# Optimization experiments

Measured on AMD Instinct MI355X. Metric: run time of the kernel, lower is better.

The kernel has to match this reference:

```python
import jax, jax.numpy as jnp
import numpy as np

HID = 256  # hardcoded LSTM hidden size in the module


def _lstm_cell(x, h, c, W_ih, W_hh, b_ih, b_hh):
    # PyTorch gate order: i, f, g, o. x,h: [1,HID]; W_*: [4H,HID]; b_*: [4H]
    gates = x @ W_ih.T + h @ W_hh.T + b_ih + b_hh  # [1,4H]
    i, f, g, o = jnp.split(gates, 4, axis=-1)
    c_new = jax.nn.sigmoid(f) * c + jax.nn.sigmoid(i) * jnp.tanh(g)
    h_new = jax.nn.sigmoid(o) * jnp.tanh(c_new)
    return h_new, c_new


def setup_inputs() -> dict:
    key = jax.random.key(0)
    ks = jax.random.split(key, 9)
    s = 0.05
    return {
        "zm_1": jax.random.normal(ks[0], (1, HID), jnp.float32) * s,
        "W_ih": jax.random.normal(ks[1], (4 * HID, HID), jnp.float32) * s,
        "W_hh": jax.random.normal(ks[2], (4 * HID, HID), jnp.float32) * s,
        "b_ih": jax.random.normal(ks[3], (4 * HID,), jnp.float32) * s,
        "b_hh": jax.random.normal(ks[4], (4 * HID,), jnp.float32) * s,
        "W_loc": jax.random.normal(ks[5], (64, HID), jnp.float32) * s,
        "b_loc": jax.random.normal(ks[6], (64,), jnp.float32) * s,
        "W_scale": jax.random.normal(ks[7], (64, HID), jnp.float32) * s,
        "b_scale": jax.random.normal(ks[8], (64,), jnp.float32) * s,
        "K": 7,
        "batch_size": 32768,
    }


def reference(zm_1, W_ih, W_hh, b_ih, b_hh, W_loc, b_loc, W_scale, b_scale, K, batch_size):
    zm_size = W_loc.shape[0]
    h0 = jnp.zeros((1, HID), zm_1.dtype)
    c0 = jnp.zeros((1, HID), zm_1.dtype)

    def step(carry, _):
        x, h, c = carry
        h_new, c_new = _lstm_cell(x, h, c, W_ih, W_hh, b_ih, b_hh)
        # LSTM output z == h_new; it is also the next step's input
        return (h_new, h_new, c_new), h_new

    _, zs = jax.lax.scan(step, (zm_1, h0, c0), None, length=K - 1)  # [K-1,1,HID]
    p_z = jnp.concatenate([zm_1[None], zs], axis=0).reshape(K, HID)  # [K,HID]

    loc = p_z @ W_loc.T + b_loc        # [K,zm]
    scale = p_z @ W_scale.T + b_scale  # [K,zm]
    # repeat over batch dim -> [K*batch_size, zm]
    loc = jnp.broadcast_to(loc[:, None, :], (K, batch_size, zm_size)).reshape(-1, zm_size)
    scale = jnp.broadcast_to(scale[:, None, :], (K, batch_size, zm_size)).reshape(-1, zm_size)
    return loc, scale
```

## Files before the change

### kernel.cpp

```cpp
#include <hip/hip_runtime.h>
#include <cstdint>
#include <cstddef>

#define HID    256
#define NROW   1024
#define KSTEPS 7
#define ZM     64
#define BATCH  32768

typedef float f32x4 __attribute__((ext_vector_type(4)));

#define WS_GATES 0
#define WS_C     (6 * NROW)
#define WS_PZ    (6 * NROW + 7 * HID)
#define WS_TAB   (6 * NROW + 14 * HID)
#define WS_WSUM  (6 * NROW + 14 * HID + 896)

__device__ __forceinline__ float sigf(float x)       { return 1.0f / (1.0f + __expf(-x)); }
__device__ __forceinline__ float tanhf_fast(float x) { return 1.0f - 2.0f / (__expf(2.0f * x) + 1.0f); }

__device__ __forceinline__ float dot4(f32x4 a, f32x4 b) {
    return a.x * b.x + a.y * b.y + a.z * b.z + a.w * b.w;
}

__global__ __launch_bounds__(256) void init_kernel(
    const float* __restrict__ zm1,
    const float* __restrict__ Wih, const float* __restrict__ Whh,
    const float* __restrict__ bih, const float* __restrict__ bhh,
    float* __restrict__ ws)
{
    const int t = threadIdx.x, b = blockIdx.x;
    f32x4*       wsum4 = (f32x4*)(ws + WS_WSUM);
    const f32x4* a4    = (const f32x4*)Wih;
    const f32x4* c4    = (const f32x4*)Whh;
    const int id = b * 256 + t;
    wsum4[id] = a4[id] + c4[id];

    if (b == 0) {
        ws[WS_PZ + t] = zm1[t];
        ws[WS_C + t]  = 0.0f;
    }
    if (b < 64) {
        const int row = b * 16 + (t >> 4);
        const int l16 = t & 15;
        const f32x4* w4 = (const f32x4*)(Wih + (size_t)row * HID);
        const f32x4* x4 = (const f32x4*)zm1;
        float part = 0.f;
        #pragma unroll
        for (int kk = 0; kk < 4; ++kk) part += dot4(w4[l16 * 4 + kk], x4[l16 * 4 + kk]);
        part += __shfl_xor(part, 1);
        part += __shfl_xor(part, 2);
        part += __shfl_xor(part, 4);
        part += __shfl_xor(part, 8);
        if (l16 == 0) ws[WS_GATES + row] = part + bih[row] + bhh[row];
    }
}

__global__ __launch_bounds__(256) void step_kernel(
    const float* __restrict__ bih, const float* __restrict__ bhh,
    float* __restrict__ ws, int s)
{
    __shared__ float hsh[HID];
    const int t = threadIdx.x, b = blockIdx.x;
    {
        const float* gp = ws + WS_GATES + (size_t)(s - 1) * NROW;
        float gi = gp[t], gf = gp[HID + t], gg = gp[2 * HID + t], go = gp[3 * HID + t];
        float cp = ws[WS_C + (size_t)(s - 1) * HID + t];
        float cn = sigf(gf) * cp + sigf(gi) * tanhf_fast(gg);
        float h  = sigf(go) * tanhf_fast(cn);
        ws[WS_C + (size_t)s * HID + t] = cn;
        if (b == 0) ws[WS_PZ + (size_t)s * HID + t] = h;
        hsh[t] = h;
    }
    __syncthreads();
    const int row = b * 16 + (t >> 4);
    const int l16 = t & 15;
    const f32x4* w4 = (const f32x4*)(ws + WS_WSUM + (size_t)row * HID);
    const f32x4* h4 = (const f32x4*)hsh;
    float part = 0.f;
    #pragma unroll
    for (int kk = 0; kk < 4; ++kk) part += dot4(w4[l16 * 4 + kk], h4[l16 * 4 + kk]);
    part += __shfl_xor(part, 1);
    part += __shfl_xor(part, 2);
    part += __shfl_xor(part, 4);
    part += __shfl_xor(part, 8);
    if (l16 == 0) ws[WS_GATES + (size_t)s * NROW + row] = part + bih[row] + bhh[row];
}

__global__ __launch_bounds__(256) void final_kernel(
    const float* __restrict__ Wloc, const float* __restrict__ bloc,
    const float* __restrict__ Wsc,  const float* __restrict__ bsc,
    float* __restrict__ ws)
{
    __shared__ float hsh[HID];
    const int t = threadIdx.x, b = blockIdx.x;
    {
        const float* gp = ws + WS_GATES + (size_t)5 * NROW;
        float gi = gp[t], gf = gp[HID + t], gg = gp[2 * HID + t], go = gp[3 * HID + t];
        float cp = ws[WS_C + (size_t)5 * HID + t];
        float cn = sigf(gf) * cp + sigf(gi) * tanhf_fast(gg);
        hsh[t] = sigf(go) * tanhf_fast(cn);
    }
    __syncthreads();
    const int wm    = b;
    const int which = wm / KSTEPS;
    const int m     = wm % KSTEPS;
    const int j     = t >> 2;
    const int q     = t & 3;
    const float* W  = which ? Wsc : Wloc;
    const float  bb = which ? bsc[j] : bloc[j];
    const f32x4* w4 = (const f32x4*)(W + (size_t)j * HID);
    const f32x4* p4 = (m == 6) ? (const f32x4*)hsh
                               : (const f32x4*)(ws + WS_PZ + (size_t)m * HID);
    float acc = 0.f;
    #pragma unroll
    for (int kk = 0; kk < 16; ++kk) acc += dot4(w4[q * 16 + kk], p4[q * 16 + kk]);
    acc += __shfl_xor(acc, 1);
    acc += __shfl_xor(acc, 2);
    if (q == 0) ws[WS_TAB + wm * ZM + j] = acc + bb;
}

__global__ __launch_bounds__(256) void bcast_kernel(
    const float* __restrict__ tab, f32x4* __restrict__ out)
{
    const int bid   = blockIdx.x;
    const int wm    = bid >> 7;
    const int chunk = bid & 127;
    const f32x4* t4 = (const f32x4*)tab;
    const f32x4 v = t4[wm * 16 + (threadIdx.x & 15)];
    size_t base = (size_t)wm * (BATCH * ZM / 4) + (size_t)chunk * 4096 + threadIdx.x;
    #pragma unroll
    for (int k = 0; k < 16; ++k) {
        __builtin_nontemporal_store(v, &out[base + (size_t)k * 256]);
    }
}

extern "C" void kernel_launch(void* const* d_in, const int* in_sizes, int n_in,
                              void* d_out, int out_size, void* d_ws, size_t ws_size,
                              hipStream_t stream) {
    const float* zm1  = (const float*)d_in[0];
    const float* Wih  = (const float*)d_in[1];
    const float* Whh  = (const float*)d_in[2];
    const float* bih  = (const float*)d_in[3];
    const float* bhh  = (const float*)d_in[4];
    const float* Wloc = (const float*)d_in[5];
    const float* bloc = (const float*)d_in[6];
    const float* Wsc  = (const float*)d_in[7];
    const float* bsc  = (const float*)d_in[8];
    float* ws = (float*)d_ws;

    init_kernel<<<256, 256, 0, stream>>>(zm1, Wih, Whh, bih, bhh, ws);
    for (int s = 1; s <= 5; ++s)
        step_kernel<<<64, 256, 0, stream>>>(bih, bhh, ws, s);
    final_kernel<<<14, 256, 0, stream>>>(Wloc, bloc, Wsc, bsc, ws);
    bcast_kernel<<<14 * 128, 256, 0, stream>>>(ws + WS_TAB, (f32x4*)d_out);
}
```

Before: 165.0 us.

## Overlap output broadcast with serial LSTM steps by fusing projection and bcast

Result: no change. 167.5 us (+1.6%).

```diff
diff --git a/kernel.cpp b/kernel.cpp
--- a/kernel.cpp
+++ b/kernel.cpp
@@ -7,14 +7,14 @@
 #define KSTEPS 7
 #define ZM     64
 #define BATCH  32768
+#define WMSZ   (BATCH * ZM)
 
 typedef float f32x4 __attribute__((ext_vector_type(4)));
 
 #define WS_GATES 0
 #define WS_C     (6 * NROW)
-#define WS_PZ    (6 * NROW + 7 * HID)
-#define WS_TAB   (6 * NROW + 14 * HID)
-#define WS_WSUM  (6 * NROW + 14 * HID + 896)
+#define WS_TAB   (6 * NROW + 7 * HID)
+#define WS_WSUM  (6 * NROW + 7 * HID + 896)
 
 __device__ __forceinline__ float sigf(float x)       { return 1.0f / (1.0f + __expf(-x)); }
 __device__ __forceinline__ float tanhf_fast(float x) { return 1.0f - 2.0f / (__expf(2.0f * x) + 1.0f); }
@@ -23,23 +23,41 @@
     return a.x * b.x + a.y * b.y + a.z * b.z + a.w * b.w;
 }
 
-__global__ __launch_bounds__(256) void init_kernel(
+__device__ __forceinline__ void bcast_wm(const float* __restrict__ tab,
+                                         f32x4* __restrict__ out,
+                                         int wm, int chunk, int t) {
+    const f32x4* t4 = (const f32x4*)tab;
+    const f32x4 v = t4[wm * 16 + (t & 15)];
+    size_t base = (size_t)wm * (WMSZ / 4) + (size_t)chunk * 4096 + t;
+    #pragma unroll
+    for (int k = 0; k < 16; ++k)
+        __builtin_nontemporal_store(v, &out[base + (size_t)k * 256]);
+}
+
+__device__ __forceinline__ void project_row(const float* __restrict__ W,
+                                            const float* __restrict__ bvec,
+                                            const float* p, float* __restrict__ tab,
+                                            int wm, int t) {
+    const int j = t >> 2, q = t & 3;
+    const f32x4* w4 = (const f32x4*)(W + (size_t)j * HID);
+    const f32x4* p4 = (const f32x4*)p;
+    float acc = 0.f;
+    #pragma unroll
+    for (int kk = 0; kk < 16; ++kk) acc += dot4(w4[q * 16 + kk], p4[q * 16 + kk]);
+    acc += __shfl_xor(acc, 1);
+    acc += __shfl_xor(acc, 2);
+    if (q == 0) tab[wm * ZM + j] = acc + bvec[j];
+}
+
+__global__ __launch_bounds__(256) void k_init(
     const float* __restrict__ zm1,
     const float* __restrict__ Wih, const float* __restrict__ Whh,
     const float* __restrict__ bih, const float* __restrict__ bhh,
+    const float* __restrict__ Wloc, const float* __restrict__ bloc,
+    const float* __restrict__ Wsc,  const float* __restrict__ bsc,
     float* __restrict__ ws)
 {
     const int t = threadIdx.x, b = blockIdx.x;
-    f32x4*       wsum4 = (f32x4*)(ws + WS_WSUM);
-    const f32x4* a4    = (const f32x4*)Wih;
-    const f32x4* c4    = (const f32x4*)Whh;
-    const int id = b * 256 + t;
-    wsum4[id] = a4[id] + c4[id];
-
-    if (b == 0) {
-        ws[WS_PZ + t] = zm1[t];
-        ws[WS_C + t]  = 0.0f;
-    }
     if (b < 64) {
         const int row = b * 16 + (t >> 4);
         const int l16 = t & 15;
@@ -53,86 +71,88 @@
         part += __shfl_xor(part, 4);
         part += __shfl_xor(part, 8);
         if (l16 == 0) ws[WS_GATES + row] = part + bih[row] + bhh[row];
+    } else if (b < 66) {
+        const int which = b - 64;
+        project_row(which ? Wsc : Wloc, which ? bsc : bloc, zm1,
+                    ws + WS_TAB, which * KSTEPS + 0, t);
+    } else {
+        const int id = (b - 66) * 256 + t;
+        ((f32x4*)(ws + WS_WSUM))[id] = ((const f32x4*)Wih)[id] + ((const f32x4*)Whh)[id];
     }
 }
 
-__global__ __launch_bounds__(256) void step_kernel(
+__global__ __launch_bounds__(256) void k_step(
     const float* __restrict__ bih, const float* __restrict__ bhh,
-    float* __restrict__ ws, int s)
+    const float* __restrict__ Wloc, const float* __restrict__ bloc,
+    const float* __restrict__ Wsc,  const float* __restrict__ bsc,
+    float* __restrict__ ws, f32x4* __restrict__ out, int s)
 {
     __shared__ float hsh[HID];
     const int t = threadIdx.x, b = blockIdx.x;
-    {
+    if (b < 66) {
         const float* gp = ws + WS_GATES + (size_t)(s - 1) * NROW;
         float gi = gp[t], gf = gp[HID + t], gg = gp[2 * HID + t], go = gp[3 * HID + t];
-        float cp = ws[WS_C + (size_t)(s - 1) * HID + t];
+        float cp = (s == 1) ? 0.f : ws[WS_C + (size_t)(s - 1) * HID + t];
         float cn = sigf(gf) * cp + sigf(gi) * tanhf_fast(gg);
         float h  = sigf(go) * tanhf_fast(cn);
-        ws[WS_C + (size_t)s * HID + t] = cn;
-        if (b == 0) ws[WS_PZ + (size_t)s * HID + t] = h;
+        if (b == 0) ws[WS_C + (size_t)s * HID + t] = cn;
         hsh[t] = h;
+        __syncthreads();
+        if (b < 64) {
+            const int row = b * 16 + (t >> 4);
+            const int l16 = t & 15;
+            const f32x4* w4 = (const f32x4*)(ws + WS_WSUM + (size_t)row * HID);
+            const f32x4* h4 = (const f32x4*)hsh;
+            float part = 0.f;
+            #pragma unroll
+            for (int kk = 0; kk < 4; ++kk) part += dot4(w4[l16 * 4 + kk], h4[l16 * 4 + kk]);
+            part += __shfl_xor(part, 1);
+            part += __shfl_xor(part, 2);
+            part += __shfl_xor(part, 4);
+            part += __shfl_xor(part, 8);
+            if (l16 == 0) ws[WS_GATES + (size_t)s * NROW + row] = part + bih[row] + bhh[row];
+        } else {
+            const int which = b - 64;
+            project_row(which ? Wsc : Wloc, which ? bsc : bloc, hsh,
+                        ws + WS_TAB, which * KSTEPS + s, t);
+        }
+    } else {
+        const int bb = b - 66;
+        const int wm = (bb >> 7) * KSTEPS + (s - 1);
+        bcast_wm(ws + WS_TAB, out, wm, bb & 127, t);
     }
-    __syncthreads();
-    const int row = b * 16 + (t >> 4);
-    const int l16 = t & 15;
-    const f32x4* w4 = (const f32x4*)(ws + WS_WSUM + (size_t)row * HID);
-    const f32x4* h4 = (const f32x4*)hsh;
-    float part = 0.f;
-    #pragma unroll
-    for (int kk = 0; kk < 4; ++kk) part += dot4(w4[l16 * 4 + kk], h4[l16 * 4 + kk]);
-    part += __shfl_xor(part, 1);
-    part += __shfl_xor(part, 2);
-    part += __shfl_xor(part, 4);
-    part += __shfl_xor(part, 8);
-    if (l16 == 0) ws[WS_GATES + (size_t)s * NROW + row] = part + bih[row] + bhh[row];
 }
 
-__global__ __launch_bounds__(256) void final_kernel(
+__global__ __launch_bounds__(256) void k_six(
     const float* __restrict__ Wloc, const float* __restrict__ bloc,
     const float* __restrict__ Wsc,  const float* __restrict__ bsc,
-    float* __restrict__ ws)
+    float* __restrict__ ws, f32x4* __restrict__ out)
 {
     __shared__ float hsh[HID];
     const int t = threadIdx.x, b = blockIdx.x;
-    {
+    if (b < 2) {
         const float* gp = ws + WS_GATES + (size_t)5 * NROW;
         float gi = gp[t], gf = gp[HID + t], gg = gp[2 * HID + t], go = gp[3 * HID + t];
         float cp = ws[WS_C + (size_t)5 * HID + t];
         float cn = sigf(gf) * cp + sigf(gi) * tanhf_fast(gg);
         hsh[t] = sigf(go) * tanhf_fast(cn);
+        __syncthreads();
+        const int which = b;
+        project_row(which ? Wsc : Wloc, which ? bsc : bloc, hsh,
+                    ws + WS_TAB, which * KSTEPS + 6, t);
+    } else {
+        const int bb = b - 2;
+        const int wm = (bb >> 7) * KSTEPS + 5;
+        bcast_wm(ws + WS_TAB, out, wm, bb & 127, t);
     }
-    __syncthreads();
-    const int wm    = b;
-    const int which = wm / KSTEPS;
-    const int m     = wm % KSTEPS;
-    const int j     = t >> 2;
-    const int q     = t & 3;
-    const float* W  = which ? Wsc : Wloc;
-    const float  bb = which ? bsc[j] : bloc[j];
-    const f32x4* w4 = (const f32x4*)(W + (size_t)j * HID);
-    const f32x4* p4 = (m == 6) ? (const f32x4*)hsh
-                               : (const f32x4*)(ws + WS_PZ + (size_t)m * HID);
-    float acc = 0.f;
-    #pragma unroll
-    for (int kk = 0; kk < 16; ++kk) acc += dot4(w4[q * 16 + kk], p4[q * 16 + kk]);
-    acc += __shfl_xor(acc, 1);
-    acc += __shfl_xor(acc, 2);
-    if (q == 0) ws[WS_TAB + wm * ZM + j] = acc + bb;
 }
 
-__global__ __launch_bounds__(256) void bcast_kernel(
+__global__ __launch_bounds__(256) void k_bcast6(
     const float* __restrict__ tab, f32x4* __restrict__ out)
 {
-    const int bid   = blockIdx.x;
-    const int wm    = bid >> 7;
-    const int chunk = bid & 127;
-    const f32x4* t4 = (const f32x4*)tab;
-    const f32x4 v = t4[wm * 16 + (threadIdx.x & 15)];
-    size_t base = (size_t)wm * (BATCH * ZM / 4) + (size_t)chunk * 4096 + threadIdx.x;
-    #pragma unroll
-    for (int k = 0; k < 16; ++k) {
-        __builtin_nontemporal_store(v, &out[base + (size_t)k * 256]);
-    }
+    const int b = blockIdx.x;
+    const int wm = (b >> 7) * KSTEPS + 6;
+    bcast_wm(tab, out, wm, b & 127, threadIdx.x);
 }
 
 extern "C" void kernel_launch(void* const* d_in, const int* in_sizes, int n_in,
@@ -148,10 +168,11 @@
     const float* Wsc  = (const float*)d_in[7];
     const float* bsc  = (const float*)d_in[8];
     float* ws = (float*)d_ws;
+    f32x4* out = (f32x4*)d_out;
 
-    init_kernel<<<256, 256, 0, stream>>>(zm1, Wih, Whh, bih, bhh, ws);
+    k_init<<<322, 256, 0, stream>>>(zm1, Wih, Whh, bih, bhh, Wloc, bloc, Wsc, bsc, ws);
     for (int s = 1; s <= 5; ++s)
-        step_kernel<<<64, 256, 0, stream>>>(bih, bhh, ws, s);
-    final_kernel<<<14, 256, 0, stream>>>(Wloc, bloc, Wsc, bsc, ws);
-    bcast_kernel<<<14 * 128, 256, 0, stream>>>(ws + WS_TAB, (f32x4*)d_out);
+        k_step<<<322, 256, 0, stream>>>(bih, bhh, Wloc, bloc, Wsc, bsc, ws, out, s);
+    k_six<<<258, 256, 0, stream>>>(Wloc, bloc, Wsc, bsc, ws, out);
+    k_bcast6<<<256, 256, 0, stream>>>(ws + WS_TAB, out);
 }
```
